# Kernel optimization log

Hardware: AMD Instinct MI355X
Metric: run time of the kernel (lower is better)

Reference implementation:

```python
import jax, jax.numpy as jnp
import numpy as np
from jax import lax

B, N, CIN, COUT, R, K = 4, 16384, 64, 128, 32, 3
VOX_EPS = 1e-6
BN3D_EPS = 1e-4
BN1D_EPS = 1e-5
LRELU_SLOPE = 0.1


def setup_inputs() -> dict:
    key = jax.random.key(0)
    ks = jax.random.split(key, 20)
    d = {}
    d['features'] = jax.random.normal(ks[0], (B, N, CIN), jnp.float32)
    d['coords'] = jax.random.normal(ks[1], (B, N, 3), jnp.float32)
    # Conv3D #1: (D,H,W,Cin,Cout) + bias
    d['conv1_w'] = jax.random.normal(ks[2], (K, K, K, CIN, COUT), jnp.float32) * 0.02
    d['conv1_b'] = jax.random.normal(ks[3], (COUT,), jnp.float32) * 0.02
    d['bn1_g'] = jax.random.uniform(ks[4], (COUT,), jnp.float32, 0.75, 1.25)
    d['bn1_b'] = jax.random.normal(ks[5], (COUT,), jnp.float32) * 0.1
    d['bn1_m'] = jax.random.normal(ks[6], (COUT,), jnp.float32) * 0.1
    d['bn1_v'] = jax.random.uniform(ks[7], (COUT,), jnp.float32, 0.5, 1.5)
    # Conv3D #2
    d['conv2_w'] = jax.random.normal(ks[8], (K, K, K, COUT, COUT), jnp.float32) * 0.02
    d['conv2_b'] = jax.random.normal(ks[9], (COUT,), jnp.float32) * 0.02
    d['bn2_g'] = jax.random.uniform(ks[10], (COUT,), jnp.float32, 0.75, 1.25)
    d['bn2_b'] = jax.random.normal(ks[11], (COUT,), jnp.float32) * 0.1
    d['bn2_m'] = jax.random.normal(ks[12], (COUT,), jnp.float32) * 0.1
    d['bn2_v'] = jax.random.uniform(ks[13], (COUT,), jnp.float32, 0.5, 1.5)
    # Point SharedMLP: Conv1D k=1 -> matmul, + BN + ReLU
    d['pw'] = jax.random.normal(ks[14], (CIN, COUT), jnp.float32) * 0.05
    d['pb'] = jax.random.normal(ks[15], (COUT,), jnp.float32) * 0.02
    d['pbn_g'] = jax.random.uniform(ks[16], (COUT,), jnp.float32, 0.75, 1.25)
    d['pbn_b'] = jax.random.normal(ks[17], (COUT,), jnp.float32) * 0.1
    d['pbn_m'] = jax.random.normal(ks[18], (COUT,), jnp.float32) * 0.1
    d['pbn_v'] = jax.random.uniform(ks[19], (COUT,), jnp.float32, 0.5, 1.5)
    return d


def _bn(x, g, b, m, v, eps):
    return (x - m) * (g * lax.rsqrt(v + eps)) + b


def _leaky_relu(x):
    return jnp.where(x >= 0, x, LRELU_SLOPE * x)


def _pvconv(features, coords, conv1_w, conv1_b, bn1_g, bn1_b, bn1_m, bn1_v,
            conv2_w, conv2_b, bn2_g, bn2_b, bn2_m, bn2_v,
            pw, pb, pbn_g, pbn_b, pbn_m, pbn_v):
    r = R
    # ---- Voxelization (normalize coords, scatter-average into grid) ----
    c = lax.stop_gradient(coords)                                   # (B,N,3)
    nc = c - jnp.mean(c, axis=1, keepdims=True)
    denom = jnp.max(jnp.linalg.norm(nc, axis=2, keepdims=True), axis=1, keepdims=True) * 2.0 + VOX_EPS
    nc = nc / denom + 0.5
    nc = jnp.clip(nc * r, 0.0, r - 1)                                # (B,N,3) in [0, r-1]
    vox = jnp.round(nc).astype(jnp.int32)                            # (B,N,3)

    batch_off = jnp.arange(B, dtype=jnp.int32)[:, None] * (r * r * r)
    lin = batch_off + vox[..., 0] * (r * r) + vox[..., 1] * r + vox[..., 2]  # (B,N)
    lin = lin.reshape(-1)
    feat_flat = features.reshape(-1, CIN)
    sums = jax.ops.segment_sum(feat_flat, lin, num_segments=B * r * r * r)   # (B*r^3,Cin)
    cnts = jax.ops.segment_sum(jnp.ones((B * N,), jnp.float32), lin, num_segments=B * r * r * r)
    cnts = jnp.where(cnts == 0, 1.0, cnts)
    grid = (sums / cnts[:, None]).reshape(B, r, r, r, CIN)           # (B,r,r,r,Cin)

    # ---- Voxel branch: Conv3D -> BN -> LeakyReLU (x2) ----
    dn = ('NDHWC', 'DHWIO', 'NDHWC')
    g = lax.conv_general_dilated(grid, conv1_w, (1, 1, 1), 'SAME', dimension_numbers=dn) + conv1_b
    g = _leaky_relu(_bn(g, bn1_g, bn1_b, bn1_m, bn1_v, BN3D_EPS))
    g = lax.conv_general_dilated(g, conv2_w, (1, 1, 1), 'SAME', dimension_numbers=dn) + conv2_b
    g = _leaky_relu(_bn(g, bn2_g, bn2_b, bn2_m, bn2_v, BN3D_EPS))    # (B,r,r,r,Cout)

    # ---- Trilinear devoxelize: gather 8 corners with interpolation weights ----
    g_flat = g.reshape(B, r * r * r, COUT)
    c0 = jnp.floor(nc).astype(jnp.int32)                             # (B,N,3)
    frac = nc - c0.astype(nc.dtype)
    c1 = jnp.minimum(c0 + 1, r - 1)
    vox_pts = jnp.zeros((B, N, COUT), jnp.float32)
    for dx in (0, 1):
        for dy in (0, 1):
            for dz in (0, 1):
                ix = c1[..., 0] if dx else c0[..., 0]
                iy = c1[..., 1] if dy else c0[..., 1]
                iz = c1[..., 2] if dz else c0[..., 2]
                w = ((frac[..., 0] if dx else 1.0 - frac[..., 0]) *
                     (frac[..., 1] if dy else 1.0 - frac[..., 1]) *
                     (frac[..., 2] if dz else 1.0 - frac[..., 2]))   # (B,N)
                idx = ix * (r * r) + iy * r + iz                      # (B,N)
                gathered = jnp.take_along_axis(g_flat, idx[..., None], axis=1)  # (B,N,Cout)
                vox_pts = vox_pts + w[..., None] * gathered

    # ---- Point branch: SharedMLP (1x1 conv -> BN -> ReLU) ----
    pf = jnp.einsum('bnc,cd->bnd', features, pw) + pb
    pf = jax.nn.relu(_bn(pf, pbn_g, pbn_b, pbn_m, pbn_v, BN1D_EPS))

    return vox_pts + pf                                              # (B,N,Cout)


def reference(features, coords, conv1_w, conv1_b, bn1_g, bn1_b, bn1_m, bn1_v,
              conv2_w, conv2_b, bn2_g, bn2_b, bn2_m, bn2_v,
              pw, pb, pbn_g, pbn_b, pbn_m, pbn_v):
    fused = _pvconv(features, coords, conv1_w, conv1_b, bn1_g, bn1_b, bn1_m, bn1_v,
                    conv2_w, conv2_b, bn2_g, bn2_b, bn2_m, bn2_v,
                    pw, pb, pbn_g, pbn_b, pbn_m, pbn_v)
    return (fused, coords)
```

## Files before the change

kernel.cpp:

```cpp
#include <hip/hip_runtime.h>
#include <hip/hip_bf16.h>

constexpr int B    = 4;
constexpr int N    = 16384;
constexpr int CIN  = 64;
constexpr int COUT = 128;
constexpr int R    = 32;
constexpr int R3   = R * R * R;
constexpr int RP   = 34;
constexpr int RP3  = RP * RP * RP;
constexpr float VOX_EPS   = 1e-6f;
constexpr float BN3D_EPS  = 1e-4f;
constexpr float BN1D_EPS  = 1e-5f;
constexpr float LRELU     = 0.1f;

typedef __attribute__((ext_vector_type(8))) short bf16x8;
typedef __attribute__((ext_vector_type(4))) float f32x4;
typedef __attribute__((ext_vector_type(8))) unsigned short u16x8;

__device__ inline float bf2f(ushort u) {
    union { unsigned int i; float f; } x; x.i = ((unsigned int)u) << 16; return x.f;
}
__device__ inline ushort f2bf(float f) {
    union { float f; unsigned int i; } x; x.f = f;
    unsigned int r = x.i + 0x7fffu + ((x.i >> 16) & 1u);
    return (ushort)(r >> 16);
}

__device__ inline int swz(int base, int z) {
    return (base ^ (z & 3) ^ ((z >> 2) & 3)) & 3;
}

__global__ __launch_bounds__(256) void k_stats_sum(const float* __restrict__ coords,
                                                   float* __restrict__ stats) {
    int blk = blockIdx.x;
    int b = blk >> 4, stripe = blk & 15;
    const float* c = coords + ((size_t)b * N + stripe * 1024) * 3;
    float sx = 0.f, sy = 0.f, sz = 0.f;
    for (int i = threadIdx.x; i < 1024; i += 256) {
        sx += c[i * 3 + 0];
        sy += c[i * 3 + 1];
        sz += c[i * 3 + 2];
    }
    __shared__ float red[256];
    float vals[3] = {sx, sy, sz};
    for (int k = 0; k < 3; ++k) {
        red[threadIdx.x] = vals[k];
        __syncthreads();
        for (int s = 128; s > 0; s >>= 1) {
            if (threadIdx.x < s) red[threadIdx.x] += red[threadIdx.x + s];
            __syncthreads();
        }
        if (threadIdx.x == 0) atomicAdd(&stats[b * 8 + k], red[0]);
        __syncthreads();
    }
}

__global__ __launch_bounds__(256) void k_stats_max(const float* __restrict__ coords,
                                                   float* __restrict__ stats) {
    int blk = blockIdx.x;
    int b = blk >> 4, stripe = blk & 15;
    const float invN = 1.0f / (float)N;
    float mx = stats[b * 8 + 0] * invN;
    float my = stats[b * 8 + 1] * invN;
    float mz = stats[b * 8 + 2] * invN;
    const float* c = coords + ((size_t)b * N + stripe * 1024) * 3;
    float mm = 0.f;
    for (int i = threadIdx.x; i < 1024; i += 256) {
        float dx = c[i * 3 + 0] - mx;
        float dy = c[i * 3 + 1] - my;
        float dz = c[i * 3 + 2] - mz;
        mm = fmaxf(mm, sqrtf(dx * dx + dy * dy + dz * dz));
    }
    __shared__ float red[256];
    red[threadIdx.x] = mm;
    __syncthreads();
    for (int s = 128; s > 0; s >>= 1) {
        if (threadIdx.x < s) red[threadIdx.x] = fmaxf(red[threadIdx.x], red[threadIdx.x + s]);
        __syncthreads();
    }
    if (threadIdx.x == 0)
        atomicMax((unsigned*)&stats[b * 8 + 3], __float_as_uint(red[0]));
}

__device__ inline void compute_nc(const float* __restrict__ coords,
                                  const float* __restrict__ stats,
                                  int p, int b, float& nx, float& ny, float& nz) {
    const float invN = 1.0f / (float)N;
    float mmax = __uint_as_float(((const unsigned*)stats)[b * 8 + 3]);
    float denom = mmax * 2.0f + VOX_EPS;
    float cx = coords[(size_t)p * 3 + 0];
    float cy = coords[(size_t)p * 3 + 1];
    float cz = coords[(size_t)p * 3 + 2];
    nx = (cx - stats[b * 8 + 0] * invN) / denom + 0.5f;
    ny = (cy - stats[b * 8 + 1] * invN) / denom + 0.5f;
    nz = (cz - stats[b * 8 + 2] * invN) / denom + 0.5f;
    nx = fminf(fmaxf(nx * (float)R, 0.f), (float)(R - 1));
    ny = fminf(fmaxf(ny * (float)R, 0.f), (float)(R - 1));
    nz = fminf(fmaxf(nz * (float)R, 0.f), (float)(R - 1));
}

__global__ __launch_bounds__(256) void k_scatter(const float* __restrict__ coords,
                                                 const float* __restrict__ feats,
                                                 const float* __restrict__ stats,
                                                 float* __restrict__ sums,
                                                 float* __restrict__ cnt) {
    int sub = threadIdx.x >> 6;
    int ci  = threadIdx.x & 63;
    int p   = blockIdx.x * 4 + sub;
    __shared__ int s_lin[4];
    if (ci == 0) {
        int b = p >> 14;
        float nx, ny, nz;
        compute_nc(coords, stats, p, b, nx, ny, nz);
        int vx = (int)rintf(nx);
        int vy = (int)rintf(ny);
        int vz = (int)rintf(nz);
        int lin = ((b * R + vx) * R + vy) * R + vz;
        s_lin[sub] = lin;
        atomicAdd(&cnt[lin], 1.0f);
    }
    __syncthreads();
    atomicAdd(&sums[(size_t)s_lin[sub] * CIN + ci], feats[(size_t)p * CIN + ci]);
}

__global__ __launch_bounds__(256) void k_zero_border(ushort* __restrict__ buf, int nchunks) {
    int i = blockIdx.x * 256 + threadIdx.x;
    if (i >= nchunks) return;
    int v = i >> 2;
    int r = v % RP3;
    int z = r % RP;
    int t = r / RP;
    int y = t % RP;
    int x = (t / RP) % RP;
    if (x == 0 || x == RP - 1 || y == 0 || y == RP - 1 || z == 0 || z == RP - 1)
        *(uint4*)(buf + (size_t)i * 8) = make_uint4(0u, 0u, 0u, 0u);
}

__global__ __launch_bounds__(256) void k_finalize(const float* __restrict__ sums,
                                                  const float* __restrict__ cnt,
                                                  ushort* __restrict__ gridp) {
    int i = blockIdx.x * 256 + threadIdx.x;
    float c = cnt[i >> 6];
    float val = sums[i] / (c == 0.f ? 1.f : c);
    int ci = i & 63;
    int v = i >> 6;
    int vz = v & 31, vy = (v >> 5) & 31, vx = (v >> 10) & 31, b = v >> 15;
    size_t o = ((((size_t)(b * 2 + (ci >> 5)) * RP + vx + 1) * RP + vy + 1) * RP + vz + 1) * 32
               + (ci & 31);
    gridp[o] = f2bf(val);
}

__global__ __launch_bounds__(256) void k_wq(const float* __restrict__ w,
                                            ushort* __restrict__ wq) {
    int idx = blockIdx.x * 256 + threadIdx.x;
    int j    = idx & 7;
    int lane = (idx >> 3) & 63;
    int nt   = (idx >> 9) & 7;
    int g    = idx >> 12;
    int k = g * 32 + ((lane >> 4) << 3) + j;
    int n = nt * 16 + (lane & 15);
    wq[idx] = f2bf(w[(size_t)k * COUT + n]);
}

template <int CI, bool PLANAR_OUT>
__global__ __launch_bounds__(256, 3) void k_conv_mfma(const ushort* __restrict__ in,
                                                      const ushort* __restrict__ wq,
                                                      const float* __restrict__ bias,
                                                      const float* __restrict__ bng,
                                                      const float* __restrict__ bnb,
                                                      const float* __restrict__ bnm,
                                                      const float* __restrict__ bnv,
                                                      ushort* __restrict__ out) {
    constexpr int NCHI = CI / 32;
    __shared__ __align__(16) ushort sl[18 * RP * 32];

    int bid = blockIdx.x;
    int Y = bid & 7;
    int x = (bid >> 3) & 31;
    int b = bid >> 8;
    int y0 = Y * 4;
    int tid = threadIdx.x;
    int wave = tid >> 6, lane = tid & 63, quad = lane >> 4, l16 = lane & 15;

    f32x4 acc[8][2] = {};

    for (int cc = 0; cc < NCHI; ++cc) {
        const ushort* base = in + (((size_t)(b * NCHI + cc) * RP + x) * RP + y0) * RP * 32;
        __syncthreads();
        for (int t = tid; t < 18 * 136; t += 256) {
            int row = t / 136;
            int g16 = t - row * 136;
            int X = row / 6, Yl = row - X * 6;
            int z = g16 >> 2, ch = g16 & 3;
            uint4 v = *(const uint4*)(base + ((size_t)(X * RP + Yl) * RP) * 32 + g16 * 8);
            *(uint4*)(sl + ((row * RP + z) * 4 + swz(ch, z)) * 8) = v;
        }
        __syncthreads();

        const ushort* bp0 = wq + ((size_t)(cc * 8 + wave * 2) * 64 + lane) * 8;
        bf16x8 cb0 = *(const bf16x8*)bp0;
        bf16x8 cb1 = *(const bf16x8*)(bp0 + 512);
        for (int tap = 0; tap < 27; ++tap) {
            int t2 = tap < 26 ? tap + 1 : 26;
            int dx2 = t2 % 3, dyz2 = t2 / 3;
            int dz2 = dyz2 % 3, dy2 = dyz2 / 3;
            int g2 = ((dx2 * 3 + dy2) * 3 + dz2) * NCHI + cc;
            const ushort* bp = wq + ((size_t)(g2 * 8 + wave * 2) * 64 + lane) * 8;
            bf16x8 nb0 = *(const bf16x8*)bp;
            bf16x8 nb1 = *(const bf16x8*)(bp + 512);

            int dx = tap % 3, dyz = tap / 3;
            int dz = dyz % 3, dy = dyz / 3;
#pragma unroll
            for (int mt = 0; mt < 8; ++mt) {
                int i = mt >> 1;
                int zrow = (mt & 1) * 16 + l16 + dz;
                int row18 = dx * 6 + i + dy;
                bf16x8 a = *(const bf16x8*)(sl + ((row18 * RP + zrow) * 4 + swz(quad, zrow)) * 8);
                acc[mt][0] = __builtin_amdgcn_mfma_f32_16x16x32_bf16(a, cb0, acc[mt][0], 0, 0, 0);
                acc[mt][1] = __builtin_amdgcn_mfma_f32_16x16x32_bf16(a, cb1, acc[mt][1], 0, 0, 0);
            }
            cb0 = nb0; cb1 = nb1;
        }
    }

    int co0 = wave * 32 + l16;
    int co1 = co0 + 16;
    float sc0 = bng[co0] * rsqrtf(bnv[co0] + BN3D_EPS);
    float sb0 = bnb[co0] - bnm[co0] * sc0;
    float bs0 = bias[co0];
    float sc1 = bng[co1] * rsqrtf(bnv[co1] + BN3D_EPS);
    float sb1 = bnb[co1] - bnm[co1] * sc1;
    float bs1 = bias[co1];
#pragma unroll
    for (int mt = 0; mt < 8; ++mt) {
        int i = mt >> 1;
#pragma unroll
        for (int reg = 0; reg < 4; ++reg) {
            int z = (mt & 1) * 16 + quad * 4 + reg;
            float v0 = (acc[mt][0][reg] + bs0) * sc0 + sb0;
            v0 = v0 >= 0.f ? v0 : LRELU * v0;
            float v1 = (acc[mt][1][reg] + bs1) * sc1 + sb1;
            v1 = v1 >= 0.f ? v1 : LRELU * v1;
            if (PLANAR_OUT) {
                size_t o = ((((size_t)(b * 4 + wave) * RP + (x + 1)) * RP + (y0 + i + 1)) * RP
                            + (z + 1)) * 32;
                out[o + l16]      = f2bf(v0);
                out[o + 16 + l16] = f2bf(v1);
            } else {
                size_t o = (((size_t)(b * R + x) * R + (y0 + i)) * R + z) * COUT + wave * 32 + l16;
                out[o]      = f2bf(v0);
                out[o + 16] = f2bf(v1);
            }
        }
    }
}

__global__ __launch_bounds__(256, 2) void k_devox(const float* __restrict__ coords,
                                                  const float* __restrict__ feats,
                                                  const float* __restrict__ stats,
                                                  const ushort* __restrict__ g2,
                                                  const ushort* __restrict__ pwq,
                                                  const float* __restrict__ pb,
                                                  const float* __restrict__ pg,
                                                  const float* __restrict__ pbb,
                                                  const float* __restrict__ pm,
                                                  const float* __restrict__ pv,
                                                  float* __restrict__ out) {
    __shared__ __align__(16) ushort sfeat[128 * 64];
    __shared__ int   sidx[128 * 8];
    __shared__ float swt[128 * 8];

    int blk = blockIdx.x, tid = threadIdx.x;
    int wave = tid >> 6, lane = tid & 63, quad = lane >> 4, l16 = lane & 15;
    int p0 = blk * 128;

    if (tid < 128) {
        int p = p0 + tid, b = p >> 14;
        float nx, ny, nz;
        compute_nc(coords, stats, p, b, nx, ny, nz);
        int cx0 = (int)floorf(nx), cy0 = (int)floorf(ny), cz0 = (int)floorf(nz);
        float fx = nx - (float)cx0, fy = ny - (float)cy0, fz = nz - (float)cz0;
        int cx1 = min(cx0 + 1, R - 1), cy1 = min(cy0 + 1, R - 1), cz1 = min(cz0 + 1, R - 1);
#pragma unroll
        for (int k = 0; k < 8; ++k) {
            int dx = (k >> 2) & 1, dy = (k >> 1) & 1, dz = k & 1;
            int ix = dx ? cx1 : cx0;
            int iy = dy ? cy1 : cy0;
            int iz = dz ? cz1 : cz0;
            sidx[tid * 8 + k] = (((b * R + ix) * R + iy) * R + iz) * COUT;
            swt[tid * 8 + k] = (dx ? fx : 1.f - fx) * (dy ? fy : 1.f - fy) * (dz ? fz : 1.f - fz);
        }
    }
    for (int i = 0; i < 4; ++i) {
        int c = i * 256 + tid;
        int p = c >> 3, ch = c & 7;
        const float* src = feats + (size_t)(p0 + p) * CIN + ch * 8;
        float4 f0 = *(const float4*)src;
        float4 f1 = *(const float4*)(src + 4);
        u16x8 u;
        u[0] = f2bf(f0.x); u[1] = f2bf(f0.y); u[2] = f2bf(f0.z); u[3] = f2bf(f0.w);
        u[4] = f2bf(f1.x); u[5] = f2bf(f1.y); u[6] = f2bf(f1.z); u[7] = f2bf(f1.w);
        *(u16x8*)&sfeat[(p * 8 + (ch ^ (p & 7))) * 8] = u;
    }
    __syncthreads();

    f32x4 acc[8][2] = {};
#pragma unroll
    for (int cc = 0; cc < 2; ++cc) {
        const ushort* bp = pwq + ((size_t)(cc * 8 + wave * 2) * 64 + lane) * 8;
        bf16x8 b0 = *(const bf16x8*)bp;
        bf16x8 b1 = *(const bf16x8*)(bp + 512);
#pragma unroll
        for (int mt = 0; mt < 8; ++mt) {
            int prow = mt * 16 + l16;
            int ch = cc * 4 + quad;
            bf16x8 a = *(const bf16x8*)&sfeat[(prow * 8 + (ch ^ (prow & 7))) * 8];
            acc[mt][0] = __builtin_amdgcn_mfma_f32_16x16x32_bf16(a, b0, acc[mt][0], 0, 0, 0);
            acc[mt][1] = __builtin_amdgcn_mfma_f32_16x16x32_bf16(a, b1, acc[mt][1], 0, 0, 0);
        }
    }

    int co0 = wave * 32 + l16, co1 = co0 + 16;
    float sc0 = pg[co0] * rsqrtf(pv[co0] + BN1D_EPS);
    float sb0 = pbb[co0] - pm[co0] * sc0;
    float bs0 = pb[co0];
    float sc1 = pg[co1] * rsqrtf(pv[co1] + BN1D_EPS);
    float sb1 = pbb[co1] - pm[co1] * sc1;
    float bs1 = pb[co1];

#pragma unroll
    for (int mt = 0; mt < 8; ++mt) {
#pragma unroll
        for (int reg = 0; reg < 4; ++reg) {
            int pl = mt * 16 + quad * 4 + reg;
            float v0 = fmaxf((acc[mt][0][reg] + bs0) * sc0 + sb0, 0.f);
            float v1 = fmaxf((acc[mt][1][reg] + bs1) * sc1 + sb1, 0.f);
#pragma unroll
            for (int k = 0; k < 8; ++k) {
                int idx = sidx[pl * 8 + k];
                float w = swt[pl * 8 + k];
                v0 += w * bf2f(g2[(size_t)idx + co0]);
                v1 += w * bf2f(g2[(size_t)idx + co1]);
            }
            size_t o = (size_t)(p0 + pl) * COUT;
            out[o + co0] = v0;
            out[o + co1] = v1;
        }
    }
}

extern "C" void kernel_launch(void* const* d_in, const int* in_sizes, int n_in,
                              void* d_out, int out_size, void* d_ws, size_t ws_size,
                              hipStream_t stream) {
    const float* feats   = (const float*)d_in[0];
    const float* coords  = (const float*)d_in[1];
    const float* conv1_w = (const float*)d_in[2];
    const float* conv1_b = (const float*)d_in[3];
    const float* bn1_g   = (const float*)d_in[4];
    const float* bn1_b   = (const float*)d_in[5];
    const float* bn1_m   = (const float*)d_in[6];
    const float* bn1_v   = (const float*)d_in[7];
    const float* conv2_w = (const float*)d_in[8];
    const float* conv2_b = (const float*)d_in[9];
    const float* bn2_g   = (const float*)d_in[10];
    const float* bn2_b   = (const float*)d_in[11];
    const float* bn2_m   = (const float*)d_in[12];
    const float* bn2_v   = (const float*)d_in[13];
    const float* pw      = (const float*)d_in[14];
    const float* pb      = (const float*)d_in[15];
    const float* pbn_g   = (const float*)d_in[16];
    const float* pbn_b   = (const float*)d_in[17];
    const float* pbn_m   = (const float*)d_in[18];
    const float* pbn_v   = (const float*)d_in[19];

    char* p = (char*)d_ws;
    float* stats = (float*)p;                        p += 256;
    float* sums  = (float*)p;                        p += (size_t)B * R3 * CIN * 4;
    float* cnt   = (float*)p;                        p += (size_t)B * R3 * 4;
    ushort* gridp = (ushort*)p;                      p += (size_t)B * 2 * RP3 * 32 * 2;
    ushort* g1p   = (ushort*)p;                      p += (size_t)B * 4 * RP3 * 32 * 2;
    ushort* g2b   = (ushort*)p;                      p += (size_t)B * R3 * COUT * 2;
    ushort* wq1   = (ushort*)p;                      p += 54 * 4096 * 2;
    ushort* wq2   = (ushort*)p;                      p += 108 * 4096 * 2;
    ushort* pwq   = (ushort*)p;                      p += 2 * 4096 * 2;
    float*  outf  = (float*)d_out;

    hipMemsetAsync(stats, 0, 256 + ((size_t)B * R3 * CIN + (size_t)B * R3) * sizeof(float),
                   stream);
    {
        int nc1 = B * 2 * RP3 * 4;
        int nc2 = B * 4 * RP3 * 4;
        k_zero_border<<<(nc1 + 255) / 256, 256, 0, stream>>>(gridp, nc1);
        k_zero_border<<<(nc2 + 255) / 256, 256, 0, stream>>>(g1p, nc2);
    }

    k_stats_sum<<<64, 256, 0, stream>>>(coords, stats);
    k_stats_max<<<64, 256, 0, stream>>>(coords, stats);
    k_scatter<<<(B * N) / 4, 256, 0, stream>>>(coords, feats, stats, sums, cnt);
    k_finalize<<<(B * R3 * CIN) / 256, 256, 0, stream>>>(sums, cnt, gridp);

    k_wq<<<(54 * 4096) / 256, 256, 0, stream>>>(conv1_w, wq1);
    k_wq<<<(108 * 4096) / 256, 256, 0, stream>>>(conv2_w, wq2);
    k_wq<<<(2 * 4096) / 256, 256, 0, stream>>>(pw, pwq);

    k_conv_mfma<CIN, true><<<B * R * (R / 4), 256, 0, stream>>>(
        gridp, wq1, conv1_b, bn1_g, bn1_b, bn1_m, bn1_v, g1p);
    k_conv_mfma<COUT, false><<<B * R * (R / 4), 256, 0, stream>>>(
        g1p, wq2, conv2_b, bn2_g, bn2_b, bn2_m, bn2_v, g2b);

    k_devox<<<(B * N) / 128, 256, 0, stream>>>(coords, feats, stats, g2b, pwq, pb,
                                               pbn_g, pbn_b, pbn_m, pbn_v, outf);

    hipMemcpyAsync(outf + (size_t)B * N * COUT, coords, (size_t)B * N * 3 * sizeof(float),
                   hipMemcpyDeviceToDevice, stream);
}
```

Measured before the change: 399.1 us.

## Retile conv MFMA work as 2x2 wave grid with 4x4 fragment tiles

Changes the per-wave tiling of the 3D conv implicit GEMM from 128 rows x 32 output channels to a 2x2 wave grid where each wave covers 64 rows x 64 channels. Each tap now loads 4 A fragments and 4 B fragments for 16 MFMAs, instead of 8 A and 2 B. This cuts LDS reads of the activation tile per MFMA. It drops the software prefetch of the next tap's weights, which may expose global weight-load latency. The epilogue indexing is rewritten to match the new layout.

Measured after the change: 355.7 us. 10.9% less time.

```diff
diff --git a/kernel.cpp b/kernel.cpp
--- a/kernel.cpp
+++ b/kernel.cpp
@@ -182,8 +182,9 @@
     int y0 = Y * 4;
     int tid = threadIdx.x;
     int wave = tid >> 6, lane = tid & 63, quad = lane >> 4, l16 = lane & 15;
-
-    f32x4 acc[8][2] = {};
+    int wm = wave >> 1, wn = wave & 1;
+
+    f32x4 acc[4][4] = {};
 
     for (int cc = 0; cc < NCHI; ++cc) {
         const ushort* base = in + (((size_t)(b * NCHI + cc) * RP + x) * RP + y0) * RP * 32;
@@ -198,60 +199,57 @@
         }
         __syncthreads();
 
-        const ushort* bp0 = wq + ((size_t)(cc * 8 + wave * 2) * 64 + lane) * 8;
-        bf16x8 cb0 = *(const bf16x8*)bp0;
-        bf16x8 cb1 = *(const bf16x8*)(bp0 + 512);
         for (int tap = 0; tap < 27; ++tap) {
-            int t2 = tap < 26 ? tap + 1 : 26;
-            int dx2 = t2 % 3, dyz2 = t2 / 3;
-            int dz2 = dyz2 % 3, dy2 = dyz2 / 3;
-            int g2 = ((dx2 * 3 + dy2) * 3 + dz2) * NCHI + cc;
-            const ushort* bp = wq + ((size_t)(g2 * 8 + wave * 2) * 64 + lane) * 8;
-            bf16x8 nb0 = *(const bf16x8*)bp;
-            bf16x8 nb1 = *(const bf16x8*)(bp + 512);
-
-            int dx = tap % 3, dyz = tap / 3;
-            int dz = dyz % 3, dy = dyz / 3;
-#pragma unroll
-            for (int mt = 0; mt < 8; ++mt) {
-                int i = mt >> 1;
-                int zrow = (mt & 1) * 16 + l16 + dz;
-                int row18 = dx * 6 + i + dy;
-                bf16x8 a = *(const bf16x8*)(sl + ((row18 * RP + zrow) * 4 + swz(quad, zrow)) * 8);
-                acc[mt][0] = __builtin_amdgcn_mfma_f32_16x16x32_bf16(a, cb0, acc[mt][0], 0, 0, 0);
-                acc[mt][1] = __builtin_amdgcn_mfma_f32_16x16x32_bf16(a, cb1, acc[mt][1], 0, 0, 0);
+            int dx = tap / 9, rem = tap - dx * 9;
+            int dy = rem / 3, dz = rem - dy * 3;
+
+            const ushort* bp = wq + ((size_t)((tap * NCHI + cc) * 8 + wn * 4) * 64 + lane) * 8;
+            bf16x8 bfr[4], afr[4];
+#pragma unroll
+            for (int nt = 0; nt < 4; ++nt)
+                bfr[nt] = *(const bf16x8*)(bp + nt * 512);
+#pragma unroll
+            for (int mt = 0; mt < 4; ++mt) {
+                int row18 = dx * 6 + wm * 2 + (mt >> 1) + dy;
+                int zrow = ((mt & 1) << 4) + l16 + dz;
+                afr[mt] = *(const bf16x8*)(sl + ((row18 * RP + zrow) * 4 + swz(quad, zrow)) * 8);
             }
-            cb0 = nb0; cb1 = nb1;
-        }
-    }
-
-    int co0 = wave * 32 + l16;
-    int co1 = co0 + 16;
-    float sc0 = bng[co0] * rsqrtf(bnv[co0] + BN3D_EPS);
-    float sb0 = bnb[co0] - bnm[co0] * sc0;
-    float bs0 = bias[co0];
-    float sc1 = bng[co1] * rsqrtf(bnv[co1] + BN3D_EPS);
-    float sb1 = bnb[co1] - bnm[co1] * sc1;
-    float bs1 = bias[co1];
-#pragma unroll
-    for (int mt = 0; mt < 8; ++mt) {
-        int i = mt >> 1;
+#pragma unroll
+            for (int mt = 0; mt < 4; ++mt)
+#pragma unroll
+                for (int nt = 0; nt < 4; ++nt)
+                    acc[mt][nt] = __builtin_amdgcn_mfma_f32_16x16x32_bf16(
+                        afr[mt], bfr[nt], acc[mt][nt], 0, 0, 0);
+        }
+    }
+
+    float sc[4], sb[4], bs[4];
+#pragma unroll
+    for (int nt = 0; nt < 4; ++nt) {
+        int co = wn * 64 + nt * 16 + l16;
+        sc[nt] = bng[co] * rsqrtf(bnv[co] + BN3D_EPS);
+        sb[nt] = bnb[co] - bnm[co] * sc[nt];
+        bs[nt] = bias[co];
+    }
+#pragma unroll
+    for (int mt = 0; mt < 4; ++mt) {
 #pragma unroll
         for (int reg = 0; reg < 4; ++reg) {
-            int z = (mt & 1) * 16 + quad * 4 + reg;
-            float v0 = (acc[mt][0][reg] + bs0) * sc0 + sb0;
-            v0 = v0 >= 0.f ? v0 : LRELU * v0;
-            float v1 = (acc[mt][1][reg] + bs1) * sc1 + sb1;
-            v1 = v1 >= 0.f ? v1 : LRELU * v1;
-            if (PLANAR_OUT) {
-                size_t o = ((((size_t)(b * 4 + wave) * RP + (x + 1)) * RP + (y0 + i + 1)) * RP
-                            + (z + 1)) * 32;
-                out[o + l16]      = f2bf(v0);
-                out[o + 16 + l16] = f2bf(v1);
-            } else {
-                size_t o = (((size_t)(b * R + x) * R + (y0 + i)) * R + z) * COUT + wave * 32 + l16;
-                out[o]      = f2bf(v0);
-                out[o + 16] = f2bf(v1);
+            int m = wm * 64 + mt * 16 + quad * 4 + reg;
+            int i = m >> 5, z = m & 31;
+#pragma unroll
+            for (int nt = 0; nt < 4; ++nt) {
+                float v = (acc[mt][nt][reg] + bs[nt]) * sc[nt] + sb[nt];
+                v = v >= 0.f ? v : LRELU * v;
+                int co = wn * 64 + nt * 16 + l16;
+                if (PLANAR_OUT) {
+                    size_t o = ((((size_t)(b * 4 + (co >> 5)) * RP + (x + 1)) * RP
+                                 + (y0 + i + 1)) * RP + (z + 1)) * 32 + (co & 31);
+                    out[o] = f2bf(v);
+                } else {
+                    size_t o = (((size_t)(b * R + x) * R + (y0 + i)) * R + z) * COUT + co;
+                    out[o] = f2bf(v);
+                }
             }
         }
     }
```
